# Kernel optimization log

Measured on AMD Instinct MI355X. Metric: run time of the kernel, lower is better.

Reference implementation:

```python
import jax, jax.numpy as jnp
import numpy as np

UNITS = 1024
BATCH = 8192
DT = 0.1
EPS = 0.1


def setup_inputs() -> dict:
    key = jax.random.key(0)
    k1, k2, k3, k4 = jax.random.split(key, 4)
    v0 = jax.random.normal(k1, (UNITS, BATCH), dtype=jnp.float32)
    v1 = jax.random.normal(k2, (UNITS, BATCH), dtype=jnp.float32)
    # learned weights (keras 'random_normal' initializer: stddev 0.05)
    B0 = jax.random.normal(k3, (UNITS, UNITS), dtype=jnp.float32) * 0.05
    q = jax.random.normal(k4, (UNITS,), dtype=jnp.float32) * 0.05
    return {"v0": v0, "v1": v1, "B0": B0, "q": q}


def reference(v0, v1, B0, q):
    u = UNITS
    eye = jnp.eye(u, dtype=v0.dtype)
    # system matrix: [[I, B0], [-B0^T, (1 + dt/eps) I]]  -> (2u, 2u)
    A = jnp.block([[eye, B0], [-B0.T, (1.0 + DT / EPS) * eye]])
    # rhs: z1 = v0 + dt*q (q broadcast along batch), z2 = v1 + (dt/eps)*tanh(v0)
    z1 = v0 + DT * q[:, None]
    z2 = v1 + (DT / EPS) * jnp.tanh(v0)
    rhs = jnp.concatenate([z1, z2], axis=0)  # (2u, batch)
    z = jnp.linalg.solve(A, rhs)             # (2u, batch)
    return z[:u, :], z[u:, :]
```

## Files before the change

### kernel.cpp

```cpp
#include <hip/hip_runtime.h>
#include <stdint.h>

typedef unsigned short u16;
typedef __bf16 bf16x8 __attribute__((ext_vector_type(8)));
typedef float f32x4 __attribute__((ext_vector_type(4)));
typedef __attribute__((address_space(3))) void as3_void;
typedef __attribute__((address_space(1))) void as1_void;

#define NU   1024
#define NBB  8192
#define LDW  2048

#define C0 0.9513167f
#define C1 (-0.3169175f)
#define C2 0.0471891f
#define C3 (-0.00321059f)
#define C4 0.00008127825f

__device__ __forceinline__ u16 f2h(float f) {
  union { float f; uint32_t u; } c; c.f = f;
  uint32_t r = (c.u + 0x7fffu + ((c.u >> 16) & 1u)) >> 16;
  return (u16)r;
}
__device__ __forceinline__ float h2f(u16 h) {
  union { uint32_t u; float f; } c; c.u = ((uint32_t)h) << 16;
  return c.f;
}

__device__ __forceinline__ void gload16(const u16* g, u16* l) {
  __builtin_amdgcn_global_load_lds((const as1_void*)g, (as3_void*)l, 16, 0, 0);
}

__global__ void prep_b0(const float* __restrict__ B0, u16* __restrict__ B0h,
                        u16* __restrict__ B0Th, u16* __restrict__ B0Tl) {
  __shared__ float t[32][33];
  const int bx = blockIdx.x, by = blockIdx.y;
  const int x = threadIdx.x, y0 = threadIdx.y;
  #pragma unroll
  for (int yy = y0; yy < 32; yy += 8) {
    const int r = by * 32 + yy, c = bx * 32 + x;
    const float v = B0[(size_t)r * NU + c];
    t[yy][x] = v;
    B0h[(size_t)r * NU + c] = f2h(v);
  }
  __syncthreads();
  #pragma unroll
  for (int yy = y0; yy < 32; yy += 8) {
    const int r = bx * 32 + yy, c = by * 32 + x;
    const float v = t[x][yy];
    const u16 hh = f2h(v);
    B0Th[(size_t)r * NU + c] = hh;
    B0Tl[(size_t)r * NU + c] = f2h(v - h2f(hh));
  }
}

__global__ void build_zzT(const float* __restrict__ v0, const float* __restrict__ v1,
                          const float* __restrict__ q, u16* __restrict__ zzT) {
  __shared__ u16 s1[32][33], s2[32][33];
  const int bx = blockIdx.x;
  const int by = blockIdx.y;
  const int x = threadIdx.x, y0 = threadIdx.y;
  #pragma unroll
  for (int yy = y0; yy < 32; yy += 8) {
    const int i = by * 32 + yy;
    const int b = bx * 32 + x;
    const float a0 = v0[(size_t)i * NBB + b];
    const float a1 = v1[(size_t)i * NBB + b];
    s1[yy][x] = f2h(a0 + 0.1f * q[i]);
    s2[yy][x] = f2h(a1 + tanhf(a0));
  }
  __syncthreads();
  #pragma unroll
  for (int yy = y0; yy < 32; yy += 8) {
    const int b = bx * 32 + yy;
    const int i = by * 32 + x;
    zzT[(size_t)b * LDW + i]      = s1[x][yy];
    zzT[(size_t)b * LDW + NU + i] = s2[x][yy];
  }
}

__global__ void transpose_f(const u16* __restrict__ in, int ldi,
                            u16* __restrict__ out, int ldo, int flip) {
  __shared__ u16 t[32][33];
  const int bx = blockIdx.x, by = blockIdx.y;
  const int x = threadIdx.x, y0 = threadIdx.y;
  #pragma unroll
  for (int yy = y0; yy < 32; yy += 8)
    t[yy][x] = in[(size_t)(by * 32 + yy) * ldi + bx * 32 + x];
  __syncthreads();
  const u16 m = flip ? (u16)0x8000u : (u16)0;
  #pragma unroll
  for (int yy = y0; yy < 32; yy += 8)
    out[(size_t)(bx * 32 + yy) * ldo + by * 32 + x] = (u16)(t[x][yy] ^ m);
}

template<int NOPS, int PDIST, int EMODE>
__global__ __launch_bounds__(256, 1)
void gemm_s(const u16* __restrict__ A0, const u16* __restrict__ A1,
            const u16* __restrict__ Bt0, const u16* __restrict__ Bt1,
            int lda, int ldb,
            const u16* __restrict__ aux, int ldaux,
            float alpha, float beta, float gamma,
            u16* __restrict__ outH, u16* __restrict__ outL, int ldc) {
  constexpr int BK = 128;
  constexpr int NA = (NOPS >= 3) ? 2 : 1;
  constexpr int NB2 = (NOPS == 4) ? 2 : 1;
  constexpr int RA = 4;
  constexpr int LOADS = RA * (NA + NB2);
  __shared__ u16 Al[PDIST][NA][64 * BK];
  __shared__ u16 Bl[PDIST][NB2][64 * BK];

  int wg = (int)blockIdx.x;
  { wg = (wg & 7) * 32 + (wg >> 3); }
  const int tm = wg & 15, tn = wg >> 4;
  const int row0 = tm << 6, col0 = tn << 6;

  const int tid = threadIdx.x;
  const int lane = tid & 63, wid = tid >> 6;
  const int wm = wid >> 1, wn = wid & 1;
  const int r16 = lane & 15, ch = lane >> 4;

  f32x4 acc[2][2] = {};

  auto stageAll = [&](int k0, int buf) {
    #pragma unroll
    for (int h = 0; h < RA; ++h) {
      const int L = tid + (h << 8);
      const int row = L >> 4;
      const int ss = (L & 15) ^ (row & 7);
      const size_t go = (size_t)(row0 + row) * lda + (size_t)(k0 + (ss << 3));
      gload16(A0 + go, &Al[buf][0][(L & ~63) << 3]);
      if constexpr (NA == 2) gload16(A1 + go, &Al[buf][1][(L & ~63) << 3]);
    }
    #pragma unroll
    for (int h = 0; h < RA; ++h) {
      const int L = tid + (h << 8);
      const int row = L >> 4;
      const int ss = (L & 15) ^ (row & 7);
      const size_t go = (size_t)(col0 + row) * ldb + (size_t)(k0 + (ss << 3));
      gload16(Bt0 + go, &Bl[buf][0][(L & ~63) << 3]);
      if constexpr (NB2 == 2) gload16(Bt1 + go, &Bl[buf][1][(L & ~63) << 3]);
    }
  };

  const int nK = 1024 / BK;
  stageAll(0, 0);
  if constexpr (PDIST == 3) stageAll(BK, 1);

  int cur = 0;
  for (int t = 0; t < nK; ++t) {
    int bs = cur + (PDIST - 1); if (bs >= PDIST) bs -= PDIST;
    if (t + PDIST - 1 < nK) {
      stageAll((t + PDIST - 1) * BK, bs);
      if constexpr (PDIST == 2) {
        if constexpr (LOADS == 8)  asm volatile("s_waitcnt vmcnt(8)" ::: "memory");
        else if constexpr (LOADS == 12) asm volatile("s_waitcnt vmcnt(12)" ::: "memory");
        else asm volatile("s_waitcnt vmcnt(16)" ::: "memory");
      } else {
        if constexpr (LOADS == 8)  asm volatile("s_waitcnt vmcnt(16)" ::: "memory");
        else asm volatile("s_waitcnt vmcnt(24)" ::: "memory");
      }
    } else if (PDIST == 3 && t + 1 < nK) {
      if constexpr (LOADS == 8)  asm volatile("s_waitcnt vmcnt(8)" ::: "memory");
      else asm volatile("s_waitcnt vmcnt(12)" ::: "memory");
    } else {
      asm volatile("s_waitcnt vmcnt(0)" ::: "memory");
    }
    __builtin_amdgcn_sched_barrier(0);
    __builtin_amdgcn_s_barrier();
    __builtin_amdgcn_sched_barrier(0);

    #pragma unroll
    for (int kk = 0; kk < BK / 32; ++kk) {
      bf16x8 av[2], bv[2], av1[2], bv1[2];
      #pragma unroll
      for (int f = 0; f < 2; ++f) {
        const int ra = (wm << 5) + (f << 4) + r16;
        const int sa = ((kk << 2) + ch) ^ (ra & 7);
        av[f] = *(const bf16x8*)&Al[cur][0][ra * BK + (sa << 3)];
        if constexpr (NA == 2)
          av1[f] = *(const bf16x8*)&Al[cur][1][ra * BK + (sa << 3)];
        const int rb = (wn << 5) + (f << 4) + r16;
        const int sb = ((kk << 2) + ch) ^ (rb & 7);
        bv[f] = *(const bf16x8*)&Bl[cur][0][rb * BK + (sb << 3)];
        if constexpr (NB2 == 2)
          bv1[f] = *(const bf16x8*)&Bl[cur][1][rb * BK + (sb << 3)];
      }
      __builtin_amdgcn_s_setprio(1);
      #pragma unroll
      for (int fm = 0; fm < 2; ++fm)
        #pragma unroll
        for (int fn = 0; fn < 2; ++fn)
          acc[fm][fn] = __builtin_amdgcn_mfma_f32_16x16x32_bf16(av[fm], bv[fn], acc[fm][fn], 0, 0, 0);
      if constexpr (NA == 2) {
        #pragma unroll
        for (int fm = 0; fm < 2; ++fm)
          #pragma unroll
          for (int fn = 0; fn < 2; ++fn)
            acc[fm][fn] = __builtin_amdgcn_mfma_f32_16x16x32_bf16(av1[fm], bv[fn], acc[fm][fn], 0, 0, 0);
      }
      if constexpr (NB2 == 2) {
        #pragma unroll
        for (int fm = 0; fm < 2; ++fm)
          #pragma unroll
          for (int fn = 0; fn < 2; ++fn)
            acc[fm][fn] = __builtin_amdgcn_mfma_f32_16x16x32_bf16(av[fm], bv1[fn], acc[fm][fn], 0, 0, 0);
      }
      __builtin_amdgcn_s_setprio(0);
    }
    __builtin_amdgcn_sched_barrier(0);
    __builtin_amdgcn_s_barrier();
    __builtin_amdgcn_sched_barrier(0);
    ++cur; if (cur == PDIST) cur = 0;
  }

  const int rbase = row0 + (wm << 5) + ((lane >> 4) << 2);
  const int cbase = col0 + (wn << 5) + (lane & 15);
  #pragma unroll
  for (int fm = 0; fm < 2; ++fm)
    #pragma unroll
    for (int fn = 0; fn < 2; ++fn)
      #pragma unroll
      for (int j = 0; j < 4; ++j) {
        const int gr = rbase + (fm << 4) + j;
        const int gc = cbase + (fn << 4);
        const float a = acc[fm][fn][j];
        if constexpr (EMODE == 0) {
          float v = alpha * a;
          if (aux) v += beta * h2f(aux[(size_t)gr * ldaux + gc]);
          if (gamma != 0.f && gr == gc) v += gamma;
          const u16 hh = f2h(v);
          outH[(size_t)gr * ldc + gc] = hh;
          if (outL) outL[(size_t)gr * ldc + gc] = f2h(v - h2f(hh));
        } else {
          outH[(size_t)gr * ldc + gc] = f2h(a);
          float g = C4 * a + C3 * h2f(aux[(size_t)gr * ldaux + gc]);
          if (gr == gc) g += C2;
          outL[(size_t)gr * ldc + gc] = f2h(g);
        }
      }
}

__global__ __launch_bounds__(512, 2)
void gemm_apply(const u16* __restrict__ A, const u16* __restrict__ Bt,
                float* __restrict__ C, int lda, int ldb, int ldc,
                int M, int N, int K) {
  __shared__ u16 Al[2][256 * 64];
  __shared__ u16 Bl[2][256 * 64];

  const int nTm = M >> 8, nTn = N >> 8;
  const int nwg = nTm * nTn;
  int wg = (int)blockIdx.x;
  { const int c = nwg >> 3; wg = (wg & 7) * c + (wg >> 3); }
  const int tm = wg % nTm, tn = wg / nTm;
  const int row0 = tm << 8, col0 = tn << 8;

  const int tid = threadIdx.x;
  const int lane = tid & 63, wid = tid >> 6;
  const int wm = wid >> 2, wn = wid & 3;
  const int r16 = lane & 15, ch = lane >> 4;

  f32x4 acc[8][4] = {};

  auto stage = [&](const u16* __restrict__ G, int gld, int grow0, int k0, u16* lb) {
    #pragma unroll
    for (int h = 0; h < 4; ++h) {
      const int L = tid + (h << 9);
      const int row = L >> 3, seg = L & 7;
      const int ss = seg ^ (row & 7);
      gload16(G + (size_t)(grow0 + row) * gld + (size_t)(k0 + (ss << 3)),
              lb + ((L & ~63) << 3));
    }
  };

  const int nK = K >> 6;
  stage(A, lda, row0, 0, &Al[0][0]);
  stage(Bt, ldb, col0, 0, &Bl[0][0]);

  for (int t = 0; t < nK; ++t) {
    const int cur = t & 1;
    if (t + 1 < nK) {
      stage(A, lda, row0, (t + 1) << 6, &Al[cur ^ 1][0]);
      stage(Bt, ldb, col0, (t + 1) << 6, &Bl[cur ^ 1][0]);
      asm volatile("s_waitcnt vmcnt(8)" ::: "memory");
    } else {
      asm volatile("s_waitcnt vmcnt(0)" ::: "memory");
    }
    __builtin_amdgcn_sched_barrier(0);
    __builtin_amdgcn_s_barrier();
    __builtin_amdgcn_sched_barrier(0);

    #pragma unroll
    for (int kk = 0; kk < 2; ++kk) {
      bf16x8 av[8], bv[4];
      #pragma unroll
      for (int f = 0; f < 8; ++f) {
        const int ra = (wm << 7) + (f << 4) + r16;
        const int sa = ((kk << 2) + ch) ^ (ra & 7);
        av[f] = *(const bf16x8*)&Al[cur][(ra << 6) + (sa << 3)];
      }
      #pragma unroll
      for (int f = 0; f < 4; ++f) {
        const int rb = (wn << 6) + (f << 4) + r16;
        const int sb = ((kk << 2) + ch) ^ (rb & 7);
        bv[f] = *(const bf16x8*)&Bl[cur][(rb << 6) + (sb << 3)];
      }
      __builtin_amdgcn_s_setprio(1);
      #pragma unroll
      for (int fm = 0; fm < 8; ++fm)
        #pragma unroll
        for (int fn = 0; fn < 4; ++fn)
          acc[fm][fn] = __builtin_amdgcn_mfma_f32_16x16x32_bf16(av[fm], bv[fn], acc[fm][fn], 0, 0, 0);
      __builtin_amdgcn_s_setprio(0);
    }
    __builtin_amdgcn_sched_barrier(0);
    __builtin_amdgcn_s_barrier();
    __builtin_amdgcn_sched_barrier(0);
  }

  const int rbase = row0 + (wm << 7) + ((lane >> 4) << 2);
  const int cbase = col0 + (wn << 6) + (lane & 15);
  #pragma unroll
  for (int fm = 0; fm < 8; ++fm)
    #pragma unroll
    for (int fn = 0; fn < 4; ++fn)
      #pragma unroll
      for (int j = 0; j < 4; ++j) {
        const int gr = rbase + (fm << 4) + j;
        const int gc = cbase + (fn << 4);
        C[(size_t)gr * ldc + gc] = acc[fm][fn][j];
      }
}

extern "C" void kernel_launch(void* const* d_in, const int* in_sizes, int n_in,
                              void* d_out, int out_size, void* d_ws, size_t ws_size,
                              hipStream_t stream) {
  (void)in_sizes; (void)n_in; (void)out_size; (void)ws_size;
  const float* v0 = (const float*)d_in[0];
  const float* v1 = (const float*)d_in[1];
  const float* B0 = (const float*)d_in[2];
  const float* q  = (const float*)d_in[3];
  float* out = (float*)d_out;

  size_t off = 0;
  char* base = (char*)d_ws;
  auto alloc = [&](size_t bytes) -> u16* {
    char* r = base + off;
    off += (bytes + 255) & ~(size_t)255;
    return (u16*)r;
  };
  u16* zzT  = alloc((size_t)NBB * LDW * 2);
  u16* Wb   = alloc((size_t)LDW * LDW * 2);
  u16* B0h  = alloc((size_t)NU * NU * 2);
  u16* B0Th = alloc((size_t)NU * NU * 2);
  u16* B0Tl = alloc((size_t)NU * NU * 2);
  u16* Mh   = alloc((size_t)NU * NU * 2);
  u16* Ml   = alloc((size_t)NU * NU * 2);
  u16* S1   = alloc((size_t)NU * NU * 2);
  u16* S2   = alloc((size_t)NU * NU * 2);
  u16* S3   = alloc((size_t)NU * NU * 2);

  u16* WbTL = Wb;
  u16* WbTR = Wb + NU;
  u16* WbBL = Wb + (size_t)NU * LDW;
  u16* WbBR = Wb + (size_t)NU * LDW + NU;

  const u16* NH = nullptr;

  prep_b0<<<dim3(32, 32), dim3(32, 8), 0, stream>>>(B0, B0h, B0Th, B0Tl);
  build_zzT<<<dim3(NBB / 32, NU / 32), dim3(32, 8), 0, stream>>>(v0, v1, q, zzT);

  gemm_s<4,2,0><<<256, 256, 0, stream>>>(B0Th, B0Tl, B0Th, B0Tl, NU, NU,
                                         NH, NU, 1.f, 0.f, 2.f, Mh, Ml, NU);
  gemm_s<2,3,1><<<256, 256, 0, stream>>>(Mh, nullptr, Mh, nullptr, NU, NU,
                                         Mh, NU, 1.f, 0.f, 0.f, S1, S2, NU);
  gemm_s<2,3,0><<<256, 256, 0, stream>>>(S1, nullptr, S2, nullptr, NU, NU,
                                         Mh, NU, 1.f, C1, C0, S3, nullptr, NU);
  gemm_s<3,3,0><<<256, 256, 0, stream>>>(Mh, Ml, S3, nullptr, NU, NU,
                                         NH, NU, -1.f, 0.f, 1.f, S1, nullptr, NU);
  gemm_s<2,3,0><<<256, 256, 0, stream>>>(S3, nullptr, S1, nullptr, NU, NU,
                                         S3, NU, 1.f, 1.f, 0.f, WbBR, nullptr, LDW);
  gemm_s<2,3,0><<<256, 256, 0, stream>>>(B0h, nullptr, WbBR, nullptr, NU, LDW,
                                         NH, NU, -1.f, 0.f, 0.f, WbTR, nullptr, LDW);
  transpose_f<<<dim3(32, 32), dim3(32, 8), 0, stream>>>(WbTR, LDW, WbBL, LDW, 1);
  gemm_s<2,3,0><<<256, 256, 0, stream>>>(WbTR, nullptr, B0h, nullptr, LDW, NU,
                                         NH, NU, 1.f, 0.f, 1.f, WbTL, nullptr, LDW);

  gemm_apply<<<(LDW / 256) * (NBB / 256), 512, 0, stream>>>(
      Wb, zzT, out, LDW, LDW, NBB, LDW, NBB, LDW);
}
```

Measured before the change: 169.9 us.

## Fuse prep kernels, fold negated transpose into GEMM epilogue, retune BK/pipeline depth

```diff
diff --git a/kernel.cpp b/kernel.cpp
--- a/kernel.cpp
+++ b/kernel.cpp
@@ -31,70 +31,56 @@
   __builtin_amdgcn_global_load_lds((const as1_void*)g, (as3_void*)l, 16, 0, 0);
 }
 
-__global__ void prep_b0(const float* __restrict__ B0, u16* __restrict__ B0h,
-                        u16* __restrict__ B0Th, u16* __restrict__ B0Tl) {
-  __shared__ float t[32][33];
-  const int bx = blockIdx.x, by = blockIdx.y;
+__global__ void prep_fused(const float* __restrict__ B0, u16* __restrict__ B0h,
+                           u16* __restrict__ B0Th, u16* __restrict__ B0Tl,
+                           const float* __restrict__ v0, const float* __restrict__ v1,
+                           const float* __restrict__ q, u16* __restrict__ zzT) {
+  __shared__ float tf[32][33];
+  __shared__ u16 s1[32][33], s2[32][33];
   const int x = threadIdx.x, y0 = threadIdx.y;
-  #pragma unroll
-  for (int yy = y0; yy < 32; yy += 8) {
-    const int r = by * 32 + yy, c = bx * 32 + x;
-    const float v = B0[(size_t)r * NU + c];
-    t[yy][x] = v;
-    B0h[(size_t)r * NU + c] = f2h(v);
+  const int b = (int)blockIdx.x;
+  if (b < 1024) {
+    const int bx = b & 31, by = b >> 5;
+    #pragma unroll
+    for (int yy = y0; yy < 32; yy += 8) {
+      const int r = by * 32 + yy, c = bx * 32 + x;
+      const float v = B0[(size_t)r * NU + c];
+      tf[yy][x] = v;
+      B0h[(size_t)r * NU + c] = f2h(v);
+    }
+    __syncthreads();
+    #pragma unroll
+    for (int yy = y0; yy < 32; yy += 8) {
+      const int r = bx * 32 + yy, c = by * 32 + x;
+      const float v = tf[x][yy];
+      const u16 hh = f2h(v);
+      B0Th[(size_t)r * NU + c] = hh;
+      B0Tl[(size_t)r * NU + c] = f2h(v - h2f(hh));
+    }
+  } else {
+    const int b2 = b - 1024;
+    const int bx = b2 & 255, by = b2 >> 8;
+    #pragma unroll
+    for (int yy = y0; yy < 32; yy += 8) {
+      const int i = by * 32 + yy;
+      const int bb = bx * 32 + x;
+      const float a0 = v0[(size_t)i * NBB + bb];
+      const float a1 = v1[(size_t)i * NBB + bb];
+      s1[yy][x] = f2h(a0 + 0.1f * q[i]);
+      s2[yy][x] = f2h(a1 + tanhf(a0));
+    }
+    __syncthreads();
+    #pragma unroll
+    for (int yy = y0; yy < 32; yy += 8) {
+      const int bb = bx * 32 + yy;
+      const int i = by * 32 + x;
+      zzT[(size_t)bb * LDW + i]      = s1[x][yy];
+      zzT[(size_t)bb * LDW + NU + i] = s2[x][yy];
+    }
   }
-  __syncthreads();
-  #pragma unroll
-  for (int yy = y0; yy < 32; yy += 8) {
-    const int r = bx * 32 + yy, c = by * 32 + x;
-    const float v = t[x][yy];
-    const u16 hh = f2h(v);
-    B0Th[(size_t)r * NU + c] = hh;
-    B0Tl[(size_t)r * NU + c] = f2h(v - h2f(hh));
-  }
-}
-
-__global__ void build_zzT(const float* __restrict__ v0, const float* __restrict__ v1,
-                          const float* __restrict__ q, u16* __restrict__ zzT) {
-  __shared__ u16 s1[32][33], s2[32][33];
-  const int bx = blockIdx.x;
-  const int by = blockIdx.y;
-  const int x = threadIdx.x, y0 = threadIdx.y;
-  #pragma unroll
-  for (int yy = y0; yy < 32; yy += 8) {
-    const int i = by * 32 + yy;
-    const int b = bx * 32 + x;
-    const float a0 = v0[(size_t)i * NBB + b];
-    const float a1 = v1[(size_t)i * NBB + b];
-    s1[yy][x] = f2h(a0 + 0.1f * q[i]);
-    s2[yy][x] = f2h(a1 + tanhf(a0));
-  }
-  __syncthreads();
-  #pragma unroll
-  for (int yy = y0; yy < 32; yy += 8) {
-    const int b = bx * 32 + yy;
-    const int i = by * 32 + x;
-    zzT[(size_t)b * LDW + i]      = s1[x][yy];
-    zzT[(size_t)b * LDW + NU + i] = s2[x][yy];
-  }
-}
-
-__global__ void transpose_f(const u16* __restrict__ in, int ldi,
-                            u16* __restrict__ out, int ldo, int flip) {
-  __shared__ u16 t[32][33];
-  const int bx = blockIdx.x, by = blockIdx.y;
-  const int x = threadIdx.x, y0 = threadIdx.y;
-  #pragma unroll
-  for (int yy = y0; yy < 32; yy += 8)
-    t[yy][x] = in[(size_t)(by * 32 + yy) * ldi + bx * 32 + x];
-  __syncthreads();
-  const u16 m = flip ? (u16)0x8000u : (u16)0;
-  #pragma unroll
-  for (int yy = y0; yy < 32; yy += 8)
-    out[(size_t)(bx * 32 + yy) * ldo + by * 32 + x] = (u16)(t[x][yy] ^ m);
-}
-
-template<int NOPS, int PDIST, int EMODE>
+}
+
+template<int NOPS, int PDIST, int BK, int EMODE>
 __global__ __launch_bounds__(256, 1)
 void gemm_s(const u16* __restrict__ A0, const u16* __restrict__ A1,
             const u16* __restrict__ Bt0, const u16* __restrict__ Bt1,
@@ -102,11 +88,12 @@
             const u16* __restrict__ aux, int ldaux,
             float alpha, float beta, float gamma,
             u16* __restrict__ outH, u16* __restrict__ outL, int ldc) {
-  constexpr int BK = 128;
   constexpr int NA = (NOPS >= 3) ? 2 : 1;
   constexpr int NB2 = (NOPS == 4) ? 2 : 1;
-  constexpr int RA = 4;
+  constexpr int RA = (64 * BK) / (256 * 8);
   constexpr int LOADS = RA * (NA + NB2);
+  constexpr int STEADY = LOADS * (PDIST - 1);
+  constexpr int SEGS = BK / 8;
   __shared__ u16 Al[PDIST][NA][64 * BK];
   __shared__ u16 Bl[PDIST][NB2][64 * BK];
 
@@ -126,8 +113,8 @@
     #pragma unroll
     for (int h = 0; h < RA; ++h) {
       const int L = tid + (h << 8);
-      const int row = L >> 4;
-      const int ss = (L & 15) ^ (row & 7);
+      const int row = L / SEGS;
+      const int ss = (L & (SEGS - 1)) ^ (row & 7);
       const size_t go = (size_t)(row0 + row) * lda + (size_t)(k0 + (ss << 3));
       gload16(A0 + go, &Al[buf][0][(L & ~63) << 3]);
       if constexpr (NA == 2) gload16(A1 + go, &Al[buf][1][(L & ~63) << 3]);
@@ -135,8 +122,8 @@
     #pragma unroll
     for (int h = 0; h < RA; ++h) {
       const int L = tid + (h << 8);
-      const int row = L >> 4;
-      const int ss = (L & 15) ^ (row & 7);
+      const int row = L / SEGS;
+      const int ss = (L & (SEGS - 1)) ^ (row & 7);
       const size_t go = (size_t)(col0 + row) * ldb + (size_t)(k0 + (ss << 3));
       gload16(Bt0 + go, &Bl[buf][0][(L & ~63) << 3]);
       if constexpr (NB2 == 2) gload16(Bt1 + go, &Bl[buf][1][(L & ~63) << 3]);
@@ -152,17 +139,15 @@
     int bs = cur + (PDIST - 1); if (bs >= PDIST) bs -= PDIST;
     if (t + PDIST - 1 < nK) {
       stageAll((t + PDIST - 1) * BK, bs);
-      if constexpr (PDIST == 2) {
-        if constexpr (LOADS == 8)  asm volatile("s_waitcnt vmcnt(8)" ::: "memory");
-        else if constexpr (LOADS == 12) asm volatile("s_waitcnt vmcnt(12)" ::: "memory");
-        else asm volatile("s_waitcnt vmcnt(16)" ::: "memory");
-      } else {
-        if constexpr (LOADS == 8)  asm volatile("s_waitcnt vmcnt(16)" ::: "memory");
-        else asm volatile("s_waitcnt vmcnt(24)" ::: "memory");
-      }
+      if constexpr (STEADY == 8)       asm volatile("s_waitcnt vmcnt(8)" ::: "memory");
+      else if constexpr (STEADY == 12) asm volatile("s_waitcnt vmcnt(12)" ::: "memory");
+      else if constexpr (STEADY == 16) asm volatile("s_waitcnt vmcnt(16)" ::: "memory");
+      else if constexpr (STEADY == 24) asm volatile("s_waitcnt vmcnt(24)" ::: "memory");
+      else                             asm volatile("s_waitcnt vmcnt(32)" ::: "memory");
     } else if (PDIST == 3 && t + 1 < nK) {
-      if constexpr (LOADS == 8)  asm volatile("s_waitcnt vmcnt(8)" ::: "memory");
-      else asm volatile("s_waitcnt vmcnt(12)" ::: "memory");
+      if constexpr (LOADS == 8)       asm volatile("s_waitcnt vmcnt(8)" ::: "memory");
+      else if constexpr (LOADS == 12) asm volatile("s_waitcnt vmcnt(12)" ::: "memory");
+      else                            asm volatile("s_waitcnt vmcnt(16)" ::: "memory");
     } else {
       asm volatile("s_waitcnt vmcnt(0)" ::: "memory");
     }
@@ -232,11 +217,15 @@
           const u16 hh = f2h(v);
           outH[(size_t)gr * ldc + gc] = hh;
           if (outL) outL[(size_t)gr * ldc + gc] = f2h(v - h2f(hh));
-        } else {
+        } else if constexpr (EMODE == 1) {
           outH[(size_t)gr * ldc + gc] = f2h(a);
           float g = C4 * a + C3 * h2f(aux[(size_t)gr * ldaux + gc]);
           if (gr == gc) g += C2;
           outL[(size_t)gr * ldc + gc] = f2h(g);
+        } else {
+          const u16 hh = f2h(alpha * a);
+          outH[(size_t)gr * ldc + gc] = hh;
+          outL[(size_t)gc * ldc + gr] = (u16)(hh ^ 0x8000u);
         }
       }
 }
@@ -367,24 +356,23 @@
 
   const u16* NH = nullptr;
 
-  prep_b0<<<dim3(32, 32), dim3(32, 8), 0, stream>>>(B0, B0h, B0Th, B0Tl);
-  build_zzT<<<dim3(NBB / 32, NU / 32), dim3(32, 8), 0, stream>>>(v0, v1, q, zzT);
-
-  gemm_s<4,2,0><<<256, 256, 0, stream>>>(B0Th, B0Tl, B0Th, B0Tl, NU, NU,
-                                         NH, NU, 1.f, 0.f, 2.f, Mh, Ml, NU);
-  gemm_s<2,3,1><<<256, 256, 0, stream>>>(Mh, nullptr, Mh, nullptr, NU, NU,
-                                         Mh, NU, 1.f, 0.f, 0.f, S1, S2, NU);
-  gemm_s<2,3,0><<<256, 256, 0, stream>>>(S1, nullptr, S2, nullptr, NU, NU,
-                                         Mh, NU, 1.f, C1, C0, S3, nullptr, NU);
-  gemm_s<3,3,0><<<256, 256, 0, stream>>>(Mh, Ml, S3, nullptr, NU, NU,
-                                         NH, NU, -1.f, 0.f, 1.f, S1, nullptr, NU);
-  gemm_s<2,3,0><<<256, 256, 0, stream>>>(S3, nullptr, S1, nullptr, NU, NU,
-                                         S3, NU, 1.f, 1.f, 0.f, WbBR, nullptr, LDW);
-  gemm_s<2,3,0><<<256, 256, 0, stream>>>(B0h, nullptr, WbBR, nullptr, NU, LDW,
-                                         NH, NU, -1.f, 0.f, 0.f, WbTR, nullptr, LDW);
-  transpose_f<<<dim3(32, 32), dim3(32, 8), 0, stream>>>(WbTR, LDW, WbBL, LDW, 1);
-  gemm_s<2,3,0><<<256, 256, 0, stream>>>(WbTR, nullptr, B0h, nullptr, LDW, NU,
-                                         NH, NU, 1.f, 0.f, 1.f, WbTL, nullptr, LDW);
+  prep_fused<<<1024 + NBB / 32 * (NU / 32), dim3(32, 8), 0, stream>>>(
+      B0, B0h, B0Th, B0Tl, v0, v1, q, zzT);
+
+  gemm_s<4,2,128,0><<<256, 256, 0, stream>>>(B0Th, B0Tl, B0Th, B0Tl, NU, NU,
+                                             NH, NU, 1.f, 0.f, 2.f, Mh, Ml, NU);
+  gemm_s<2,2,256,1><<<256, 256, 0, stream>>>(Mh, nullptr, Mh, nullptr, NU, NU,
+                                             Mh, NU, 1.f, 0.f, 0.f, S1, S2, NU);
+  gemm_s<2,2,256,0><<<256, 256, 0, stream>>>(S1, nullptr, S2, nullptr, NU, NU,
+                                             Mh, NU, 1.f, C1, C0, S3, nullptr, NU);
+  gemm_s<3,3,128,0><<<256, 256, 0, stream>>>(Mh, Ml, S3, nullptr, NU, NU,
+                                             NH, NU, -1.f, 0.f, 1.f, S1, nullptr, NU);
+  gemm_s<2,2,256,0><<<256, 256, 0, stream>>>(S3, nullptr, S1, nullptr, NU, NU,
+                                             S3, NU, 1.f, 1.f, 0.f, WbBR, nullptr, LDW);
+  gemm_s<2,2,256,2><<<256, 256, 0, stream>>>(B0h, nullptr, WbBR, nullptr, NU, LDW,
+                                             NH, NU, -1.f, 0.f, 0.f, WbTR, WbBL, LDW);
+  gemm_s<2,2,256,0><<<256, 256, 0, stream>>>(WbTR, nullptr, B0h, nullptr, LDW, NU,
+                                             NH, NU, 1.f, 0.f, 1.f, WbTL, nullptr, LDW);
 
   gemm_apply<<<(LDW / 256) * (NBB / 256), 512, 0, stream>>>(
       Wb, zzT, out, LDW, LDW, NBB, LDW, NBB, LDW);
```

Result: faster. 166.3 us (median of 3 runs) (-2.1%).
